# Kernel optimization log

Measured on AMD Instinct MI355X. Metric: run time of the kernel, lower is better.

Reference implementation:

```python
import jax, jax.numpy as jnp
import numpy as np

N_DOF = 7
WIDTH = 1024
BATCH = 8192
EPS = 1e-5
LSIZE = N_DOF * (N_DOF + 1) // 2   # diag (n) + strictly-lower ((n^2-n)/2)


def _tri_idx(n):
    # order matches LowTri: offset -i chunks, within-chunk j -> entry (j+i, j)
    r, c = [], []
    for i in range(n):
        for j in range(n - i):
            r.append(j + i)
            c.append(j)
    return np.array(r, np.int32), np.array(c, np.int32)

_R, _C = _tri_idx(N_DOF)


def setup_inputs() -> dict:
    key = jax.random.key(0)
    ks = jax.random.split(key, 9)

    def glorot(k, shape):
        std = (2.0 / (shape[0] + shape[1])) ** 0.5
        return (jax.random.normal(k, shape, jnp.float32) * std).astype(jnp.float32)

    lower = LSIZE - N_DOF
    b0 = 0.1
    return {
        "state": jax.random.normal(ks[0], (BATCH, N_DOF), jnp.float32),
        "velocity": jax.random.normal(ks[1], (BATCH, N_DOF), jnp.float32),
        "acceleration": jax.random.normal(ks[2], (BATCH, N_DOF), jnp.float32),
        "W_in": glorot(ks[3], (N_DOF, WIDTH)), "b_in": jnp.full((WIDTH,), b0, jnp.float32),
        "W_h": glorot(ks[4], (WIDTH, WIDTH)), "b_h": jnp.full((WIDTH,), b0, jnp.float32),
        "W_g": glorot(ks[5], (WIDTH, 1)), "b_g": jnp.full((1,), b0, jnp.float32),
        "W_ld": glorot(ks[6], (WIDTH, N_DOF)), "b_ld": jnp.full((N_DOF,), b0, jnp.float32),
        "W_lo": glorot(ks[7], (WIDTH, lower)), "b_lo": jnp.full((lower,), b0, jnp.float32),
    }


def _layer(x, der, W, b, act):
    # a: [B, out]; der: [B, in, n_dof] -> [B, out, n_dof]
    a = x @ W + b
    if act == "relu":
        y = jax.nn.relu(a)
        gp = (a > 0).astype(a.dtype)
    else:  # linear
        y = a
        gp = jnp.ones_like(a)
    # diag(g'(a)) @ W^T @ prev_der  ==  g'(a)[:, :, None] * (W^T @ prev_der)
    new_der = gp[:, :, None] * jnp.einsum("io,bid->bod", W, der)
    return y, new_der


def _forward(state, velocity, acceleration,
             W_in, b_in, W_h, b_h, W_g, b_g, W_ld, b_ld, W_lo, b_lo):
    B = state.shape[0]
    eye = jnp.broadcast_to(jnp.eye(N_DOF, dtype=state.dtype), (B, N_DOF, N_DOF))

    y1, d1 = _layer(state, eye, W_in, b_in, "relu")
    y2, d2 = _layer(y1, d1, W_h, b_h, "relu")
    y3, d3 = _layer(y2, d2, W_h, b_h, "relu")   # original reuses hidden_layer1 twice

    V, derV = _layer(y3, d3, W_g, b_g, "linear")       # derV: [B, 1, n_dof]
    l_diag, der_ld = _layer(y3, d3, W_ld, b_ld, "relu")
    l_low, der_lo = _layer(y3, d3, W_lo, b_lo, "linear")

    l = jnp.concatenate([l_diag, l_low], axis=1)          # [B, LSIZE]
    der_l = jnp.concatenate([der_ld, der_lo], axis=1)     # [B, LSIZE, n_dof]

    def lowtri(v):   # [B, LSIZE] -> [B, n, n]
        return jnp.zeros((B, N_DOF, N_DOF), v.dtype).at[:, _R, _C].set(v)

    def lowtri3d(v):  # [B, n_dof, LSIZE] -> [B, n_dof, n, n]
        return jnp.zeros((B, N_DOF, N_DOF, N_DOF), v.dtype).at[:, :, _R, _C].set(v)

    L = lowtri(l)
    LT = jnp.swapaxes(L, 1, 2)
    M = L @ LT + EPS * jnp.eye(N_DOF, dtype=L.dtype)

    dldt = jnp.einsum("bld,bd->bl", der_l, velocity)
    dLdt = lowtri(dldt)
    dMdt = L @ jnp.swapaxes(dLdt, 1, 2) + dLdt @ LT

    dLdq = lowtri3d(jnp.swapaxes(der_l, 1, 2))            # [B, n_dof, n, n]
    dMdq = dLdq @ LT[:, None] + L[:, None] @ jnp.swapaxes(dLdq, 2, 3)

    dMdt_dq = jnp.einsum("bij,bj->bi", dMdt, velocity)
    quad_dq = jnp.einsum("bi,bkij,bj->bk", velocity, dMdq, velocity)
    C = dMdt_dq - 0.5 * quad_dq
    G = derV[:, 0, :]                                      # squeeze [B,1,n_dof]
    Mddq = jnp.einsum("bij,bj->bi", M, acceleration)
    tau_pred = Mddq + C + G
    return tau_pred, M, C, G


def reference(state, velocity, acceleration,
              W_in, b_in, W_h, b_h, W_g, b_g, W_ld, b_ld, W_lo, b_lo):
    return _forward(state, velocity, acceleration,
                    W_in, b_in, W_h, b_h, W_g, b_g, W_ld, b_ld, W_lo, b_lo)
```

## Files before the change

kernel.cpp:

```cpp
#include <hip/hip_runtime.h>
#include <hip/hip_bf16.h>

#define WIDTH 1024
#define BATCH 8192

typedef __attribute__((ext_vector_type(8))) short short8;
typedef __attribute__((ext_vector_type(4))) float floatx4;

typedef __attribute__((address_space(1))) void gvoid;
typedef __attribute__((address_space(3))) void lvoid;

__device__ __forceinline__ void async_copy16(const void* g, void* l) {
    __builtin_amdgcn_global_load_lds((gvoid*)g, (lvoid*)l, 16, 0, 0);
}

__device__ __forceinline__ void split_store(float v, __hip_bfloat16* hi, __hip_bfloat16* lo, long idx) {
    __hip_bfloat16 h = __float2bfloat16(v);
    hi[idx] = h;
    lo[idx] = __float2bfloat16(v - __bfloat162float(h));
}

__global__ __launch_bounds__(256) void transpose_k(
    const float* __restrict__ W,
    __hip_bfloat16* __restrict__ Wth, __hip_bfloat16* __restrict__ Wtl)
{
    __shared__ float t[32][33];
    const int tx = threadIdx.x & 31, ty = threadIdx.x >> 5;
    const int bx = blockIdx.x << 5, by = blockIdx.y << 5;
#pragma unroll
    for (int r = 0; r < 32; r += 8)
        t[ty + r][tx] = W[(long)(by + ty + r) * WIDTH + bx + tx];
    __syncthreads();
#pragma unroll
    for (int r = 0; r < 32; r += 8)
        split_store(t[tx][ty + r], Wth, Wtl, (long)(bx + ty + r) * WIDTH + by + tx);
}

__global__ __launch_bounds__(256) void buildwcat_k(
    const float* __restrict__ W_ld, const float* __restrict__ W_lo,
    const float* __restrict__ W_g,
    __hip_bfloat16* __restrict__ Wch, __hip_bfloat16* __restrict__ Wcl)
{
    const int idx = blockIdx.x * 256 + threadIdx.x;
    const int n = idx >> 10, k = idx & 1023;
    float v = 0.f;
    if (n < 7)       v = W_ld[k * 7 + n];
    else if (n < 28) v = W_lo[k * 21 + (n - 7)];
    else if (n == 28) v = W_g[k];
    split_store(v, Wch, Wcl, idx);
}

__global__ __launch_bounds__(256) void prep_k(
    const float* __restrict__ state,
    const float* __restrict__ W_in,
    const float* __restrict__ b_in,
    __hip_bfloat16* __restrict__ Y1h, __hip_bfloat16* __restrict__ Y1l,
    __hip_bfloat16* __restrict__ D1h)
{
    const int b = blockIdx.x;
    const int j0 = threadIdx.x * 4;
    float s[7];
#pragma unroll
    for (int d = 0; d < 7; ++d) s[d] = state[b * 7 + d];
    float a[4];
#pragma unroll
    for (int q = 0; q < 4; ++q) a[q] = b_in[j0 + q];
    float w[7][4];
#pragma unroll
    for (int d = 0; d < 7; ++d)
#pragma unroll
        for (int q = 0; q < 4; ++q) {
            w[d][q] = W_in[d * WIDTH + j0 + q];
            a[q] += s[d] * w[d][q];
        }
    bool gp[4];
#pragma unroll
    for (int q = 0; q < 4; ++q) {
        gp[q] = a[q] > 0.f;
        split_store(gp[q] ? a[q] : 0.f, Y1h, Y1l, (long)b * WIDTH + j0 + q);
    }
    union { unsigned long long u64; unsigned short h[4]; } pk;
#pragma unroll
    for (int d = 0; d < 7; ++d) {
#pragma unroll
        for (int q = 0; q < 4; ++q) {
            __hip_bfloat16 v = __float2bfloat16(gp[q] ? w[d][q] : 0.f);
            pk.h[q] = *reinterpret_cast<unsigned short*>(&v);
        }
        *reinterpret_cast<unsigned long long*>(&D1h[((long)b * 7 + d) * WIDTH + j0]) = pk.u64;
    }
}

__device__ __forceinline__ void y_gemm_body(
    short* SM,
    int bm, int bn, int tid,
    const __hip_bfloat16* Ah, const __hip_bfloat16* Al,
    const __hip_bfloat16* Bh, const __hip_bfloat16* Bl,
    const float* bias,
    __hip_bfloat16* outh, __hip_bfloat16* outl)
{
    short* Ash = SM;          short* Asl = SM + 4096;
    short* Bsh = SM + 8192;   short* Bsl = SM + 12288;
    const int lane = tid & 63;
    const int wv = tid >> 6;
    const int wm = wv >> 1, wn = wv & 1;
    const int srow = tid >> 2;
    const int scol = (tid & 3) << 3;
    const short* pAh = (const short*)Ah + (long)(bm * 128 + srow) * WIDTH + scol;
    const short* pAl = (const short*)Al + (long)(bm * 128 + srow) * WIDTH + scol;
    const short* pBh = (const short*)Bh + (long)(bn * 128 + srow) * WIDTH + scol;
    const short* pBl = (const short*)Bl + (long)(bn * 128 + srow) * WIDTH + scol;
    const long half = 64l * WIDTH;

    floatx4 acc[4][4] = {};
    const int r = lane & 15;
    const int kq = (lane >> 4) << 3;

    for (int kt = 0; kt < WIDTH; kt += 32) {
        __syncthreads();
        async_copy16(pAh + kt,        Ash + wv * 512);
        async_copy16(pAh + half + kt, Ash + 2048 + wv * 512);
        async_copy16(pAl + kt,        Asl + wv * 512);
        async_copy16(pAl + half + kt, Asl + 2048 + wv * 512);
        async_copy16(pBh + kt,        Bsh + wv * 512);
        async_copy16(pBh + half + kt, Bsh + 2048 + wv * 512);
        async_copy16(pBl + kt,        Bsl + wv * 512);
        async_copy16(pBl + half + kt, Bsl + 2048 + wv * 512);
        __syncthreads();
        short8 afh[4], afl[4], bfh[4], bfl[4];
#pragma unroll
        for (int i = 0; i < 4; ++i) {
            const int ar = (wm * 64 + i * 16 + r) * 32 + kq;
            afh[i] = *reinterpret_cast<const short8*>(&Ash[ar]);
            afl[i] = *reinterpret_cast<const short8*>(&Asl[ar]);
        }
#pragma unroll
        for (int j = 0; j < 4; ++j) {
            const int br = (wn * 64 + j * 16 + r) * 32 + kq;
            bfh[j] = *reinterpret_cast<const short8*>(&Bsh[br]);
            bfl[j] = *reinterpret_cast<const short8*>(&Bsl[br]);
        }
#pragma unroll
        for (int i = 0; i < 4; ++i)
#pragma unroll
            for (int j = 0; j < 4; ++j) {
                acc[i][j] = __builtin_amdgcn_mfma_f32_16x16x32_bf16(afh[i], bfh[j], acc[i][j], 0, 0, 0);
                acc[i][j] = __builtin_amdgcn_mfma_f32_16x16x32_bf16(afh[i], bfl[j], acc[i][j], 0, 0, 0);
                acc[i][j] = __builtin_amdgcn_mfma_f32_16x16x32_bf16(afl[i], bfh[j], acc[i][j], 0, 0, 0);
            }
    }

    const int r4 = (lane >> 4) << 2;
#pragma unroll
    for (int i = 0; i < 4; ++i)
#pragma unroll
        for (int j = 0; j < 4; ++j) {
            const int col = bn * 128 + wn * 64 + j * 16 + r;
#pragma unroll
            for (int rr = 0; rr < 4; ++rr) {
                const int row = bm * 128 + wm * 64 + i * 16 + r4 + rr;
                float v = acc[i][j][rr] + bias[col];
                v = v > 0.f ? v : 0.f;
                split_store(v, outh, outl, (long)row * WIDTH + col);
            }
        }
}

__global__ __launch_bounds__(256) void gemm_y(
    const __hip_bfloat16* __restrict__ Ah, const __hip_bfloat16* __restrict__ Al,
    const __hip_bfloat16* __restrict__ Bh, const __hip_bfloat16* __restrict__ Bl,
    const float* __restrict__ bias,
    __hip_bfloat16* __restrict__ outh, __hip_bfloat16* __restrict__ outl)
{
    __shared__ __align__(16) short SM[16384];
    y_gemm_body(SM, blockIdx.x, blockIdx.y, threadIdx.x, Ah, Al, Bh, Bl, bias, outh, outl);
}


__device__ __forceinline__ void stage_chunk_d2(
    short* SMbase, const short* __restrict__ A, const short* __restrict__ B,
    int tau, int c, int tid)
{
    const short* src = (c & 1) ? B : A;
    const int kbase = (tau << 6) + ((c >> 1) << 5);
    short* region = SMbase + ((tau & 1) << 15) + (c << 13);
    const int wvb = tid & 0x1C0;
#pragma unroll
    for (int j = 0; j < 2; ++j) {
        const int idx = tid + (j << 9);
        async_copy16(src + (long)(idx >> 2) * WIDTH + kbase + ((idx & 3) << 3),
                     region + ((long)(wvb + (j << 9)) << 3));
    }
}

__global__ __launch_bounds__(512, 2) void d2y3_8p(
    const __hip_bfloat16* __restrict__ D1,
    const __hip_bfloat16* __restrict__ Wth, const __hip_bfloat16* __restrict__ Wtl,
    const __hip_bfloat16* __restrict__ Y2h, const __hip_bfloat16* __restrict__ Y2l,
    const float* __restrict__ bias,
    __hip_bfloat16* __restrict__ D2out,
    __hip_bfloat16* __restrict__ Y3h, __hip_bfloat16* __restrict__ Y3l,
    int nd2)
{
    __shared__ __align__(16) short SM[65536];
    const int tid = threadIdx.x;

    if ((int)blockIdx.x >= nd2) {
        const int half = tid >> 8;
        y_gemm_body(SM + (half << 14), blockIdx.x - nd2, blockIdx.y + (half << 2),
                    tid & 255, Y2h, Y2l, Wth, Wtl, bias, Y3h, Y3l);
        return;
    }

    const short* Abase = (const short*)D1 + (long)blockIdx.x * 256 * WIDTH;
    const short* Bbase = (const short*)Wth + (long)blockIdx.y * 256 * WIDTH;
    const int lane = tid & 63;
    const int wv = tid >> 6;
    const int wm = wv >> 2, wn = wv & 3;
    const int r = lane & 15;
    const int kq = (lane >> 4) << 3;

    floatx4 acc[8][4] = {};

    stage_chunk_d2(SM, Abase, Bbase, 0, 0, tid);
    stage_chunk_d2(SM, Abase, Bbase, 0, 1, tid);
    stage_chunk_d2(SM, Abase, Bbase, 0, 2, tid);
    stage_chunk_d2(SM, Abase, Bbase, 0, 3, tid);
    stage_chunk_d2(SM, Abase, Bbase, 1, 0, tid);
    stage_chunk_d2(SM, Abase, Bbase, 1, 1, tid);
    stage_chunk_d2(SM, Abase, Bbase, 1, 2, tid);
    asm volatile("s_waitcnt vmcnt(10)" ::: "memory");
    __builtin_amdgcn_s_barrier();

    short8 af[8], bf[2];
#pragma unroll 2
    for (int t = 0; t < 16; ++t) {
        short* buf = SM + ((t & 1) << 15);
#pragma unroll
        for (int ks = 0; ks < 2; ++ks) {
            const short* Ab = buf + (ks ? 2 : 0) * 8192;
            const short* Bb = buf + (ks ? 3 : 1) * 8192;

#pragma unroll
            for (int i = 0; i < 8; ++i)
                af[i] = *reinterpret_cast<const short8*>(&Ab[(wm * 128 + i * 16 + r) * 32 + kq]);
#pragma unroll
            for (int j = 0; j < 2; ++j)
                bf[j] = *reinterpret_cast<const short8*>(&Bb[(wn * 64 + j * 16 + r) * 32 + kq]);
            if (ks == 0) { if (t + 1 < 16) stage_chunk_d2(SM, Abase, Bbase, t + 1, 3, tid); }
            else         { if (t + 2 < 16) stage_chunk_d2(SM, Abase, Bbase, t + 2, 1, tid); }
            __builtin_amdgcn_s_barrier();
            asm volatile("s_waitcnt lgkmcnt(0)");
            __builtin_amdgcn_sched_barrier(0);
            __builtin_amdgcn_s_setprio(1);
#pragma unroll
            for (int i = 0; i < 8; ++i)
#pragma unroll
                for (int j = 0; j < 2; ++j)
                    acc[i][j] = __builtin_amdgcn_mfma_f32_16x16x32_bf16(af[i], bf[j], acc[i][j], 0, 0, 0);
            __builtin_amdgcn_s_setprio(0);
            __builtin_amdgcn_s_barrier();

#pragma unroll
            for (int j = 0; j < 2; ++j)
                bf[j] = *reinterpret_cast<const short8*>(&Bb[(wn * 64 + (2 + j) * 16 + r) * 32 + kq]);
            if (ks == 0) { if (t + 2 < 16) stage_chunk_d2(SM, Abase, Bbase, t + 2, 0, tid); }
            else         { if (t + 2 < 16) stage_chunk_d2(SM, Abase, Bbase, t + 2, 2, tid); }
            __builtin_amdgcn_s_barrier();
            asm volatile("s_waitcnt lgkmcnt(0)");
            __builtin_amdgcn_sched_barrier(0);
            __builtin_amdgcn_s_setprio(1);
#pragma unroll
            for (int i = 0; i < 8; ++i)
#pragma unroll
                for (int j = 0; j < 2; ++j)
                    acc[i][2 + j] = __builtin_amdgcn_mfma_f32_16x16x32_bf16(af[i], bf[j], acc[i][2 + j], 0, 0, 0);
            __builtin_amdgcn_s_setprio(0);
            if (ks == 0) {
                if (t < 14)       asm volatile("s_waitcnt vmcnt(10)" ::: "memory");
                else if (t == 14) asm volatile("s_waitcnt vmcnt(8)"  ::: "memory");
                else              asm volatile("s_waitcnt vmcnt(0)"  ::: "memory");
            } else {
                if (t < 14)       asm volatile("s_waitcnt vmcnt(10)" ::: "memory");
                else if (t == 14) asm volatile("s_waitcnt vmcnt(4)"  ::: "memory");
            }
            __builtin_amdgcn_s_barrier();
        }
    }

    const int r4 = (lane >> 4) << 2;
#pragma unroll
    for (int i = 0; i < 8; ++i)
#pragma unroll
        for (int j = 0; j < 4; ++j) {
            const int col = blockIdx.y * 256 + wn * 64 + j * 16 + r;
#pragma unroll
            for (int rr = 0; rr < 4; ++rr) {
                const int row = blockIdx.x * 256 + wm * 128 + i * 16 + r4 + rr;
                float v = acc[i][j][rr];
                const unsigned brow = (unsigned)row / 7u;
                if (!(__bfloat162float(Y2h[(long)brow * WIDTH + col]) > 0.f)) v = 0.f;
                D2out[(long)row * WIDTH + col] = __float2bfloat16(v);
            }
        }
}

__global__ __launch_bounds__(256) void d3heady_k(
    const __hip_bfloat16* __restrict__ D2,
    const __hip_bfloat16* __restrict__ Wth, const __hip_bfloat16* __restrict__ Wtl,
    const __hip_bfloat16* __restrict__ Y3h, const __hip_bfloat16* __restrict__ Y3l,
    const __hip_bfloat16* __restrict__ Wch, const __hip_bfloat16* __restrict__ Wcl,
    float* __restrict__ PDpart, float* __restrict__ PY,
    int nd, int Mrows)
{
    __shared__ __align__(16) short SM[26112];
    const int tid = threadIdx.x;
    const int lane = tid & 63;
    const int wv = tid >> 6;
    const int r = lane & 15;
    const int kq = (lane >> 4) << 3;
    const int r4 = (lane >> 4) << 2;
    const int srow = tid >> 2;
    const int scol = (tid & 3) << 3;
    const long half = 64l * WIDTH;

    if ((int)blockIdx.x >= nd) {
        if (blockIdx.y != 0) return;
        short* Ash = SM;          short* Asl = SM + 4096;
        short* Bsh = SM + 8192;   short* Bsl = SM + 9216;
        const int bm = blockIdx.x - nd;
        const short* pAh = (const short*)Y3h + (long)(bm * 128 + srow) * WIDTH + scol;
        const short* pAl = (const short*)Y3l + (long)(bm * 128 + srow) * WIDTH + scol;
        const long boff = (long)srow * WIDTH + scol;
        const short* pBh = (const short*)Wch;  const short* pBl = (const short*)Wcl;

        floatx4 acc[2][2] = {};
        for (int kt = 0; kt < WIDTH; kt += 32) {
            short8 gbh, gbl;
            if (tid < 128) {
                gbh = *reinterpret_cast<const short8*>(pBh + boff + kt);
                gbl = *reinterpret_cast<const short8*>(pBl + boff + kt);
            }
            __syncthreads();
            async_copy16(pAh + kt,        Ash + wv * 512);
            async_copy16(pAh + half + kt, Ash + 2048 + wv * 512);
            async_copy16(pAl + kt,        Asl + wv * 512);
            async_copy16(pAl + half + kt, Asl + 2048 + wv * 512);
            if (tid < 128) {
                *reinterpret_cast<short8*>(&Bsh[srow * 32 + scol]) = gbh;
                *reinterpret_cast<short8*>(&Bsl[srow * 32 + scol]) = gbl;
            }
            __syncthreads();
            short8 afh[2], afl[2], bfh[2], bfl[2];
#pragma unroll
            for (int i = 0; i < 2; ++i) {
                const int ar = (wv * 32 + i * 16 + r) * 32 + kq;
                afh[i] = *reinterpret_cast<const short8*>(&Ash[ar]);
                afl[i] = *reinterpret_cast<const short8*>(&Asl[ar]);
            }
#pragma unroll
            for (int j = 0; j < 2; ++j) {
                const int br = (j * 16 + r) * 32 + kq;
                bfh[j] = *reinterpret_cast<const short8*>(&Bsh[br]);
                bfl[j] = *reinterpret_cast<const short8*>(&Bsl[br]);
            }
#pragma unroll
            for (int i = 0; i < 2; ++i)
#pragma unroll
                for (int j = 0; j < 2; ++j) {
                    acc[i][j] = __builtin_amdgcn_mfma_f32_16x16x32_bf16(afh[i], bfh[j], acc[i][j], 0, 0, 0);
                    acc[i][j] = __builtin_amdgcn_mfma_f32_16x16x32_bf16(afh[i], bfl[j], acc[i][j], 0, 0, 0);
                    acc[i][j] = __builtin_amdgcn_mfma_f32_16x16x32_bf16(afl[i], bfh[j], acc[i][j], 0, 0, 0);
                }
        }
#pragma unroll
        for (int i = 0; i < 2; ++i)
#pragma unroll
            for (int j = 0; j < 2; ++j)
#pragma unroll
                for (int rr = 0; rr < 4; ++rr) {
                    const int row = bm * 128 + wv * 32 + i * 16 + r4 + rr;
                    PY[(long)row * 32 + j * 16 + r] = acc[i][j][rr];
                }
        return;
    }

    short* Ash0 = SM;         short* Ash1 = SM + 4096;
    short* Bsh0 = SM + 8192;  short* Bsh1 = SM + 12288;
    short* T    = SM;
    short* WcH  = SM + 17408;
    short* WcL  = SM + 21760;

    const int wm = wv >> 1, wn = wv & 1;
    const int bm = blockIdx.x, bn = blockIdx.y;
    const short* pAh = (const short*)D2 + (long)(bm * 128 + srow) * WIDTH + scol;
    const short* pBh = (const short*)Wth + (long)(bn * 128 + srow) * WIDTH + scol;

    floatx4 acc[4][4] = {};
    for (int kt = 0; kt < WIDTH; kt += 64) {
        __syncthreads();
        async_copy16(pAh + kt,             Ash0 + wv * 512);
        async_copy16(pAh + half + kt,      Ash0 + 2048 + wv * 512);
        async_copy16(pAh + kt + 32,        Ash1 + wv * 512);
        async_copy16(pAh + half + kt + 32, Ash1 + 2048 + wv * 512);
        async_copy16(pBh + kt,             Bsh0 + wv * 512);
        async_copy16(pBh + half + kt,      Bsh0 + 2048 + wv * 512);
        async_copy16(pBh + kt + 32,        Bsh1 + wv * 512);
        async_copy16(pBh + half + kt + 32, Bsh1 + 2048 + wv * 512);
        __syncthreads();
#pragma unroll
        for (int s = 0; s < 2; ++s) {
            const short* As = s ? Ash1 : Ash0;
            const short* Bs = s ? Bsh1 : Bsh0;
            short8 afh[4], bfh[4];
#pragma unroll
            for (int i = 0; i < 4; ++i)
                afh[i] = *reinterpret_cast<const short8*>(&As[(wm * 64 + i * 16 + r) * 32 + kq]);
#pragma unroll
            for (int j = 0; j < 4; ++j)
                bfh[j] = *reinterpret_cast<const short8*>(&Bs[(wn * 64 + j * 16 + r) * 32 + kq]);
#pragma unroll
            for (int i = 0; i < 4; ++i)
#pragma unroll
                for (int j = 0; j < 4; ++j)
                    acc[i][j] = __builtin_amdgcn_mfma_f32_16x16x32_bf16(afh[i], bfh[j], acc[i][j], 0, 0, 0);
        }
    }

    __syncthreads();
#pragma unroll
    for (int i = 0; i < 4; ++i)
#pragma unroll
        for (int j = 0; j < 4; ++j) {
            const int coll = wn * 64 + j * 16 + r;
            const int colg = bn * 128 + coll;
#pragma unroll
            for (int rr = 0; rr < 4; ++rr) {
                const int rowl = wm * 64 + i * 16 + r4 + rr;
                const int rowg = bm * 128 + rowl;
                float v = acc[i][j][rr];
                const unsigned brow = (unsigned)rowg / 7u;
                if (!(__bfloat162float(Y3h[(long)brow * WIDTH + colg]) > 0.f)) v = 0.f;
                __hip_bfloat16 hb = __float2bfloat16(v);
                T[rowl * 136 + coll] = *reinterpret_cast<short*>(&hb);
            }
        }
    {
        const int n = tid >> 4, k8 = (tid & 15) * 8;
        const short* wh = (const short*)Wch;
        const short* wl = (const short*)Wcl;
        *reinterpret_cast<short8*>(&WcH[n * 136 + k8]) =
            *reinterpret_cast<const short8*>(wh + n * WIDTH + bn * 128 + k8);
        *reinterpret_cast<short8*>(&WcH[(n + 16) * 136 + k8]) =
            *reinterpret_cast<const short8*>(wh + (n + 16) * WIDTH + bn * 128 + k8);
        *reinterpret_cast<short8*>(&WcL[n * 136 + k8]) =
            *reinterpret_cast<const short8*>(wl + n * WIDTH + bn * 128 + k8);
        *reinterpret_cast<short8*>(&WcL[(n + 16) * 136 + k8]) =
            *reinterpret_cast<const short8*>(wl + (n + 16) * WIDTH + bn * 128 + k8);
    }
    __syncthreads();

    floatx4 accp[2][2] = {};
#pragma unroll
    for (int kk = 0; kk < 128; kk += 32) {
        short8 af[2], bh8[2], bl8[2];
#pragma unroll
        for (int i = 0; i < 2; ++i)
            af[i] = *reinterpret_cast<const short8*>(&T[(wv * 32 + i * 16 + r) * 136 + kk + kq]);
#pragma unroll
        for (int j = 0; j < 2; ++j) {
            bh8[j] = *reinterpret_cast<const short8*>(&WcH[(j * 16 + r) * 136 + kk + kq]);
            bl8[j] = *reinterpret_cast<const short8*>(&WcL[(j * 16 + r) * 136 + kk + kq]);
        }
#pragma unroll
        for (int i = 0; i < 2; ++i)
#pragma unroll
            for (int j = 0; j < 2; ++j) {
                accp[i][j] = __builtin_amdgcn_mfma_f32_16x16x32_bf16(af[i], bh8[j], accp[i][j], 0, 0, 0);
                accp[i][j] = __builtin_amdgcn_mfma_f32_16x16x32_bf16(af[i], bl8[j], accp[i][j], 0, 0, 0);
            }
    }
#pragma unroll
    for (int i = 0; i < 2; ++i)
#pragma unroll
        for (int j = 0; j < 2; ++j)
#pragma unroll
            for (int rr = 0; rr < 4; ++rr) {
                const int rowg = bm * 128 + wv * 32 + i * 16 + r4 + rr;
                PDpart[((long)bn * Mrows + rowg) * 32 + j * 16 + r] = accp[i][j][rr];
            }
}

__device__ __forceinline__ int midx(int rr, int cc) {
    const int i = rr - cc;
    return i * 7 - (i * (i - 1)) / 2 + cc;
}

__global__ __launch_bounds__(64) void finalize_k(
    const float* __restrict__ PY,
    const float* __restrict__ PDpart,
    const float* __restrict__ vel_g,
    const float* __restrict__ acc_g,
    const float* __restrict__ b_ld,
    const float* __restrict__ b_lo,
    float* __restrict__ out,
    int b0, int Mrows)
{
    __shared__ float lval[28];
    __shared__ int gpv[7];
    __shared__ float derl[29 * 7];
    __shared__ float Lm[49], Mm[49], dLt[49], uu[49];
    __shared__ float wvv[7], pv[7], Cv[7], Gv[7], tauv[7], vl[7], ac[7];

    const int bl = blockIdx.x, tid = threadIdx.x;
    const int b = b0 + bl;
    if (tid < 28) {
        float s = PY[(long)bl * 32 + tid];
        if (tid < 7) {
            s += b_ld[tid];
            gpv[tid] = s > 0.f;
            lval[tid] = s > 0.f ? s : 0.f;
        } else {
            lval[tid] = s + b_lo[tid - 7];
        }
    }
    if (tid >= 28 && tid < 35) {
        vl[tid - 28] = vel_g[b * 7 + tid - 28];
        ac[tid - 28] = acc_g[b * 7 + tid - 28];
    }
    __syncthreads();
    for (int idx = tid; idx < 203; idx += 64) {
        const int m = idx / 7, d = idx % 7;
        float v = 0.f;
#pragma unroll
        for (int p = 0; p < 8; ++p)
            v += PDpart[((long)p * Mrows + bl * 7 + d) * 32 + m];
        if (m < 7 && !gpv[m]) v = 0.f;
        derl[m * 7 + d] = v;
    }
    __syncthreads();
    if (tid < 49) {
        const int rr = tid / 7, cc = tid % 7;
        Lm[tid] = (rr >= cc) ? lval[midx(rr, cc)] : 0.f;
    }
    __syncthreads();
    if (tid < 49) {
        const int rr = tid / 7, cc = tid % 7;
        float s = 0.f;
        for (int k = 0; k < 7; ++k) s += Lm[rr * 7 + k] * Lm[cc * 7 + k];
        if (rr == cc) s += 1e-5f;
        Mm[tid] = s;
        float t = 0.f;
        if (rr >= cc) {
            const int m = midx(rr, cc);
            for (int d = 0; d < 7; ++d) t += derl[m * 7 + d] * vl[d];
        }
        dLt[tid] = t;
        float u = 0.f;
        for (int r2 = cc; r2 < 7; ++r2) u += vl[r2] * derl[midx(r2, cc) * 7 + rr];
        uu[tid] = u;
    } else if (tid >= 49 && tid < 56) {
        const int j = tid - 49;
        float s = 0.f;
        for (int r2 = 0; r2 < 7; ++r2) s += Lm[r2 * 7 + j] * vl[r2];
        wvv[j] = s;
    }
    __syncthreads();
    if (tid < 7) {
        float s = 0.f;
        for (int r2 = 0; r2 < 7; ++r2) s += dLt[r2 * 7 + tid] * vl[r2];
        pv[tid] = s;
    }
    __syncthreads();
    if (tid < 7) {
        float s = 0.f, q = 0.f, md = 0.f;
        for (int c = 0; c < 7; ++c) {
            s += Lm[tid * 7 + c] * pv[c] + dLt[tid * 7 + c] * wvv[c];
            q += uu[tid * 7 + c] * wvv[c];
            md += Mm[tid * 7 + c] * ac[c];
        }
        Cv[tid] = s - q;
        Gv[tid] = derl[28 * 7 + tid];
        tauv[tid] = md + Cv[tid] + Gv[tid];
    }
    __syncthreads();
    if (tid < 49) out[57344 + (long)b * 49 + tid] = Mm[tid];
    if (tid < 7) {
        out[(long)b * 7 + tid] = tauv[tid];
        out[458752 + (long)b * 7 + tid] = Cv[tid];
        out[516096 + (long)b * 7 + tid] = Gv[tid];
    }
}

extern "C" void kernel_launch(void* const* d_in, const int* in_sizes, int n_in,
                              void* d_out, int out_size, void* d_ws, size_t ws_size,
                              hipStream_t stream)
{
    const float* state = (const float*)d_in[0];
    const float* vel   = (const float*)d_in[1];
    const float* accel = (const float*)d_in[2];
    const float* W_in  = (const float*)d_in[3];
    const float* b_in  = (const float*)d_in[4];
    const float* W_h   = (const float*)d_in[5];
    const float* b_h   = (const float*)d_in[6];
    const float* W_g   = (const float*)d_in[7];
    const float* W_ld  = (const float*)d_in[9];
    const float* b_ld  = (const float*)d_in[10];
    const float* W_lo  = (const float*)d_in[11];
    const float* b_lo  = (const float*)d_in[12];
    float* outp = (float*)d_out;

    char* ws = (char*)d_ws;
    __hip_bfloat16* Wth = (__hip_bfloat16*)ws; ws += (size_t)WIDTH * WIDTH * 2;
    __hip_bfloat16* Wtl = (__hip_bfloat16*)ws; ws += (size_t)WIDTH * WIDTH * 2;
    __hip_bfloat16* Wch = (__hip_bfloat16*)ws; ws += 32 * WIDTH * 2;
    __hip_bfloat16* Wcl = (__hip_bfloat16*)ws; ws += 32 * WIDTH * 2;
    const size_t fixed = (size_t)(ws - (char*)d_ws);

    int CH = 256;
    for (int cand = 8192; cand >= 256; cand >>= 1) {
        size_t need = fixed + (size_t)cand * 37120;
        if (need <= ws_size) { CH = cand; break; }
    }
    const int NCH = BATCH / CH;

    const size_t YB = (size_t)CH * WIDTH * 2;
    const size_t DB = (size_t)CH * 7 * WIDTH * 2;
    __hip_bfloat16* Yah = (__hip_bfloat16*)ws; ws += YB;
    __hip_bfloat16* Yal = (__hip_bfloat16*)ws; ws += YB;
    __hip_bfloat16* Ybh = (__hip_bfloat16*)ws; ws += YB;
    __hip_bfloat16* Ybl = (__hip_bfloat16*)ws; ws += YB;
    __hip_bfloat16* Dah = (__hip_bfloat16*)ws; ws += DB;
    __hip_bfloat16* Dbh = (__hip_bfloat16*)ws; ws += DB;
    float* PY = (float*)ws; ws += (size_t)CH * 32 * 4;
    float* PDpart = (float*)Dah;

    const int Mrows = CH * 7;
    const int nd = Mrows / 128;
    const int ny = CH / 128;
    const int nd2 = Mrows / 256;

    transpose_k<<<dim3(32, 32), dim3(256), 0, stream>>>(W_h, Wth, Wtl);
    buildwcat_k<<<dim3(128), dim3(256), 0, stream>>>(W_ld, W_lo, W_g, Wch, Wcl);

    for (int c = 0; c < NCH; ++c) {
        prep_k<<<dim3(CH), dim3(256), 0, stream>>>(state + (size_t)c * CH * 7, W_in, b_in,
                                                   Yah, Yal, Dah);
        gemm_y<<<dim3(ny, 8), dim3(256), 0, stream>>>(
            Yah, Yal, Wth, Wtl, b_h, Ybh, Ybl);
        d2y3_8p<<<dim3(nd2 + ny, 4), dim3(512), 0, stream>>>(
            Dah, Wth, Wtl, Ybh, Ybl, b_h, Dbh, Yah, Yal, nd2);
        d3heady_k<<<dim3(nd + ny, 8), dim3(256), 0, stream>>>(
            Dbh, Wth, Wtl, Yah, Yal, Wch, Wcl, PDpart, PY, nd, Mrows);
        finalize_k<<<dim3(CH), dim3(64), 0, stream>>>(PY, PDpart, vel, accel, b_ld, b_lo,
                                                      outp, c * CH, Mrows);
    }
    (void)in_sizes; (void)n_in; (void)out_size;
}
```

Measured before the change: 671.6 us.

## Pipeline Y GEMMs with 512-thread double-buffered tiles and merge D3 into 256-row kernel

Replaces the 256-thread Y GEMM with a 512-thread, 128x256 tile body that double-buffers hi/lo operand chunks in LDS using async loads, explicit vmcnt waits, barriers and setprio around MFMA groups. The D3 derivative GEMM reuses the deeper 256-row pipelined D2 GEMM path, which halves the number of partial PD slices that finalize must sum. The head GEMM is split into two halves per 512-thread block. The aim is to hide global-to-LDS latency and raise MFMA utilisation. The cost is more LDS per block and hand-tuned wait counts that are fragile.

```diff
diff --git a/kernel.cpp b/kernel.cpp
--- a/kernel.cpp
+++ b/kernel.cpp
@@ -18,6 +18,16 @@
     __hip_bfloat16 h = __float2bfloat16(v);
     hi[idx] = h;
     lo[idx] = __float2bfloat16(v - __bfloat162float(h));
+}
+
+template<int N> __device__ __forceinline__ void waitv() {
+    if constexpr (N == 0)      asm volatile("s_waitcnt vmcnt(0)" ::: "memory");
+    else if constexpr (N == 1) asm volatile("s_waitcnt vmcnt(1)" ::: "memory");
+    else if constexpr (N == 3) asm volatile("s_waitcnt vmcnt(3)" ::: "memory");
+    else if constexpr (N == 6) asm volatile("s_waitcnt vmcnt(6)" ::: "memory");
+    else if constexpr (N == 7) asm volatile("s_waitcnt vmcnt(7)" ::: "memory");
+    else if constexpr (N == 8) asm volatile("s_waitcnt vmcnt(8)" ::: "memory");
+    else if constexpr (N == 9) asm volatile("s_waitcnt vmcnt(9)" ::: "memory");
 }
 
 __global__ __launch_bounds__(256) void transpose_k(
@@ -91,71 +101,122 @@
     }
 }
 
-__device__ __forceinline__ void y_gemm_body(
+
+__device__ __forceinline__ void st128(const short* src, short* region, int tid, int kbase) {
+    async_copy16(src + (long)(tid >> 2) * WIDTH + kbase + ((tid & 3) << 3),
+                 region + ((tid & 0x1C0) << 3));
+}
+__device__ __forceinline__ void st256(const short* src, short* region, int tid, int kbase) {
+#pragma unroll
+    for (int j = 0; j < 2; ++j) {
+        const int idx = tid + (j << 9);
+        async_copy16(src + (long)(idx >> 2) * WIDTH + kbase + ((idx & 3) << 3),
+                     region + (((tid & 0x1C0) + (j << 9)) << 3));
+    }
+}
+
+template<int W0, int W1, int W2, int IS>
+__device__ __forceinline__ void y8_triple(
+    short* buf, short* nbuf,
+    const short* pAh, const short* pAl, const short* pBh, const short* pBl,
+    int t, int tid, int wm, int wn, int r, int kq, floatx4 (&acc)[4][4])
+{
+    short8 fah[4], fbh[4];
+#pragma unroll
+    for (int i = 0; i < 4; ++i)
+        fah[i] = *reinterpret_cast<const short8*>(&buf[(wm * 64 + i * 16 + r) * 32 + kq]);
+#pragma unroll
+    for (int j = 0; j < 4; ++j)
+        fbh[j] = *reinterpret_cast<const short8*>(&buf[8192 + (wn * 64 + j * 16 + r) * 32 + kq]);
+    if (IS >= 1) st128(pAl, nbuf + 4096, tid, (t + 1) * 32);
+    __builtin_amdgcn_s_barrier();
+    asm volatile("s_waitcnt lgkmcnt(0)");
+    __builtin_amdgcn_sched_barrier(0);
+    __builtin_amdgcn_s_setprio(1);
+#pragma unroll
+    for (int i = 0; i < 4; ++i)
+#pragma unroll
+        for (int j = 0; j < 4; ++j)
+            acc[i][j] = __builtin_amdgcn_mfma_f32_16x16x32_bf16(fah[i], fbh[j], acc[i][j], 0, 0, 0);
+    __builtin_amdgcn_s_setprio(0);
+    waitv<W0>();
+    __builtin_amdgcn_s_barrier();
+    short8 fbl[4];
+#pragma unroll
+    for (int j = 0; j < 4; ++j)
+        fbl[j] = *reinterpret_cast<const short8*>(&buf[16384 + (wn * 64 + j * 16 + r) * 32 + kq]);
+    if (IS >= 2) { st128(pAh, buf, tid, (t + 2) * 32); st256(pBh, buf + 8192, tid, (t + 2) * 32); }
+    __builtin_amdgcn_s_barrier();
+    asm volatile("s_waitcnt lgkmcnt(0)");
+    __builtin_amdgcn_sched_barrier(0);
+    __builtin_amdgcn_s_setprio(1);
+#pragma unroll
+    for (int i = 0; i < 4; ++i)
+#pragma unroll
+        for (int j = 0; j < 4; ++j)
+            acc[i][j] = __builtin_amdgcn_mfma_f32_16x16x32_bf16(fah[i], fbl[j], acc[i][j], 0, 0, 0);
+    __builtin_amdgcn_s_setprio(0);
+    waitv<W1>();
+    __builtin_amdgcn_s_barrier();
+    short8 fal[4];
+#pragma unroll
+    for (int i = 0; i < 4; ++i)
+        fal[i] = *reinterpret_cast<const short8*>(&buf[4096 + (wm * 64 + i * 16 + r) * 32 + kq]);
+    if (IS >= 2) st256(pBl, buf + 16384, tid, (t + 2) * 32);
+    __builtin_amdgcn_s_barrier();
+    asm volatile("s_waitcnt lgkmcnt(0)");
+    __builtin_amdgcn_sched_barrier(0);
+    __builtin_amdgcn_s_setprio(1);
+#pragma unroll
+    for (int i = 0; i < 4; ++i)
+#pragma unroll
+        for (int j = 0; j < 4; ++j)
+            acc[i][j] = __builtin_amdgcn_mfma_f32_16x16x32_bf16(fal[i], fbh[j], acc[i][j], 0, 0, 0);
+    __builtin_amdgcn_s_setprio(0);
+    waitv<W2>();
+    __builtin_amdgcn_s_barrier();
+}
+
+__device__ __forceinline__ void y8_gemm_body(
     short* SM,
     int bm, int bn, int tid,
-    const __hip_bfloat16* Ah, const __hip_bfloat16* Al,
-    const __hip_bfloat16* Bh, const __hip_bfloat16* Bl,
+    const __hip_bfloat16* Ah_, const __hip_bfloat16* Al_,
+    const __hip_bfloat16* Bh_, const __hip_bfloat16* Bl_,
     const float* bias,
     __hip_bfloat16* outh, __hip_bfloat16* outl)
 {
-    short* Ash = SM;          short* Asl = SM + 4096;
-    short* Bsh = SM + 8192;   short* Bsl = SM + 12288;
-    const int lane = tid & 63;
-    const int wv = tid >> 6;
-    const int wm = wv >> 1, wn = wv & 1;
-    const int srow = tid >> 2;
-    const int scol = (tid & 3) << 3;
-    const short* pAh = (const short*)Ah + (long)(bm * 128 + srow) * WIDTH + scol;
-    const short* pAl = (const short*)Al + (long)(bm * 128 + srow) * WIDTH + scol;
-    const short* pBh = (const short*)Bh + (long)(bn * 128 + srow) * WIDTH + scol;
-    const short* pBl = (const short*)Bl + (long)(bn * 128 + srow) * WIDTH + scol;
-    const long half = 64l * WIDTH;
+    const int lane = tid & 63, wv = tid >> 6;
+    const int wm = wv >> 2, wn = wv & 3;
+    const int r = lane & 15, kq = (lane >> 4) << 3, r4 = (lane >> 4) << 2;
+    const short* pAh = (const short*)Ah_ + (long)bm * 128 * WIDTH;
+    const short* pAl = (const short*)Al_ + (long)bm * 128 * WIDTH;
+    const short* pBh = (const short*)Bh_ + (long)bn * 256 * WIDTH;
+    const short* pBl = (const short*)Bl_ + (long)bn * 256 * WIDTH;
 
     floatx4 acc[4][4] = {};
-    const int r = lane & 15;
-    const int kq = (lane >> 4) << 3;
-
-    for (int kt = 0; kt < WIDTH; kt += 32) {
-        __syncthreads();
-        async_copy16(pAh + kt,        Ash + wv * 512);
-        async_copy16(pAh + half + kt, Ash + 2048 + wv * 512);
-        async_copy16(pAl + kt,        Asl + wv * 512);
-        async_copy16(pAl + half + kt, Asl + 2048 + wv * 512);
-        async_copy16(pBh + kt,        Bsh + wv * 512);
-        async_copy16(pBh + half + kt, Bsh + 2048 + wv * 512);
-        async_copy16(pBl + kt,        Bsl + wv * 512);
-        async_copy16(pBl + half + kt, Bsl + 2048 + wv * 512);
-        __syncthreads();
-        short8 afh[4], afl[4], bfh[4], bfl[4];
-#pragma unroll
-        for (int i = 0; i < 4; ++i) {
-            const int ar = (wm * 64 + i * 16 + r) * 32 + kq;
-            afh[i] = *reinterpret_cast<const short8*>(&Ash[ar]);
-            afl[i] = *reinterpret_cast<const short8*>(&Asl[ar]);
-        }
+
+    st128(pAh, SM + 0,     tid, 0);
+    st256(pBh, SM + 8192,  tid, 0);
+    st256(pBl, SM + 16384, tid, 0);
+    st128(pAl, SM + 4096,  tid, 0);
+    st128(pAh, SM + 24576 + 0,     tid, 32);
+    st256(pBh, SM + 24576 + 8192,  tid, 32);
+    st256(pBl, SM + 24576 + 16384, tid, 32);
+    waitv<8>();
+    __builtin_amdgcn_s_barrier();
+
+    for (int t2 = 0; t2 < 15; ++t2) {
+        y8_triple<7, 9, 8, 2>(SM,         SM + 24576, pAh, pAl, pBh, pBl, 2 * t2,     tid, wm, wn, r, kq, acc);
+        y8_triple<7, 9, 8, 2>(SM + 24576, SM,         pAh, pAl, pBh, pBl, 2 * t2 + 1, tid, wm, wn, r, kq, acc);
+    }
+    y8_triple<7, 6, 3, 1>(SM,         SM + 24576, pAh, pAl, pBh, pBl, 30, tid, wm, wn, r, kq, acc);
+    y8_triple<1, 0, 0, 0>(SM + 24576, SM,         pAh, pAl, pBh, pBl, 31, tid, wm, wn, r, kq, acc);
+
+#pragma unroll
+    for (int i = 0; i < 4; ++i)
 #pragma unroll
         for (int j = 0; j < 4; ++j) {
-            const int br = (wn * 64 + j * 16 + r) * 32 + kq;
-            bfh[j] = *reinterpret_cast<const short8*>(&Bsh[br]);
-            bfl[j] = *reinterpret_cast<const short8*>(&Bsl[br]);
-        }
-#pragma unroll
-        for (int i = 0; i < 4; ++i)
-#pragma unroll
-            for (int j = 0; j < 4; ++j) {
-                acc[i][j] = __builtin_amdgcn_mfma_f32_16x16x32_bf16(afh[i], bfh[j], acc[i][j], 0, 0, 0);
-                acc[i][j] = __builtin_amdgcn_mfma_f32_16x16x32_bf16(afh[i], bfl[j], acc[i][j], 0, 0, 0);
-                acc[i][j] = __builtin_amdgcn_mfma_f32_16x16x32_bf16(afl[i], bfh[j], acc[i][j], 0, 0, 0);
-            }
-    }
-
-    const int r4 = (lane >> 4) << 2;
-#pragma unroll
-    for (int i = 0; i < 4; ++i)
-#pragma unroll
-        for (int j = 0; j < 4; ++j) {
-            const int col = bn * 128 + wn * 64 + j * 16 + r;
+            const int col = bn * 256 + wn * 64 + j * 16 + r;
 #pragma unroll
             for (int rr = 0; rr < 4; ++rr) {
                 const int row = bm * 128 + wm * 64 + i * 16 + r4 + rr;
@@ -166,16 +227,15 @@
         }
 }
 
-__global__ __launch_bounds__(256) void gemm_y(
+__global__ __launch_bounds__(512, 2) void gemm_y8(
     const __hip_bfloat16* __restrict__ Ah, const __hip_bfloat16* __restrict__ Al,
     const __hip_bfloat16* __restrict__ Bh, const __hip_bfloat16* __restrict__ Bl,
     const float* __restrict__ bias,
     __hip_bfloat16* __restrict__ outh, __hip_bfloat16* __restrict__ outl)
 {
-    __shared__ __align__(16) short SM[16384];
-    y_gemm_body(SM, blockIdx.x, blockIdx.y, threadIdx.x, Ah, Al, Bh, Bl, bias, outh, outl);
-}
-
+    __shared__ __align__(16) short SM[49152];
+    y8_gemm_body(SM, blockIdx.x, blockIdx.y, threadIdx.x, Ah, Al, Bh, Bl, bias, outh, outl);
+}
 
 __device__ __forceinline__ void stage_chunk_d2(
     short* SMbase, const short* __restrict__ A, const short* __restrict__ B,
@@ -193,35 +253,10 @@
     }
 }
 
-__global__ __launch_bounds__(512, 2) void d2y3_8p(
-    const __hip_bfloat16* __restrict__ D1,
-    const __hip_bfloat16* __restrict__ Wth, const __hip_bfloat16* __restrict__ Wtl,
-    const __hip_bfloat16* __restrict__ Y2h, const __hip_bfloat16* __restrict__ Y2l,
-    const float* __restrict__ bias,
-    __hip_bfloat16* __restrict__ D2out,
-    __hip_bfloat16* __restrict__ Y3h, __hip_bfloat16* __restrict__ Y3l,
-    int nd2)
-{
-    __shared__ __align__(16) short SM[65536];
-    const int tid = threadIdx.x;
-
-    if ((int)blockIdx.x >= nd2) {
-        const int half = tid >> 8;
-        y_gemm_body(SM + (half << 14), blockIdx.x - nd2, blockIdx.y + (half << 2),
-                    tid & 255, Y2h, Y2l, Wth, Wtl, bias, Y3h, Y3l);
-        return;
-    }
-
-    const short* Abase = (const short*)D1 + (long)blockIdx.x * 256 * WIDTH;
-    const short* Bbase = (const short*)Wth + (long)blockIdx.y * 256 * WIDTH;
-    const int lane = tid & 63;
-    const int wv = tid >> 6;
-    const int wm = wv >> 2, wn = wv & 3;
-    const int r = lane & 15;
-    const int kq = (lane >> 4) << 3;
-
-    floatx4 acc[8][4] = {};
-
+__device__ __forceinline__ void d_gemm_256(
+    short* SM, const short* Abase, const short* Bbase, int tid,
+    int wm, int wn, int r, int kq, floatx4 (&acc)[8][4])
+{
     stage_chunk_d2(SM, Abase, Bbase, 0, 0, tid);
     stage_chunk_d2(SM, Abase, Bbase, 0, 1, tid);
     stage_chunk_d2(SM, Abase, Bbase, 0, 2, tid);
@@ -287,6 +322,33 @@
             __builtin_amdgcn_s_barrier();
         }
     }
+}
+
+__global__ __launch_bounds__(512, 2) void d2y3_8p(
+    const __hip_bfloat16* __restrict__ D1,
+    const __hip_bfloat16* __restrict__ Wth, const __hip_bfloat16* __restrict__ Wtl,
+    const __hip_bfloat16* __restrict__ Y2h, const __hip_bfloat16* __restrict__ Y2l,
+    const float* __restrict__ bias,
+    __hip_bfloat16* __restrict__ D2out,
+    __hip_bfloat16* __restrict__ Y3h, __hip_bfloat16* __restrict__ Y3l,
+    int nd2)
+{
+    __shared__ __align__(16) short SM[65536];
+    const int tid = threadIdx.x;
+
+    if ((int)blockIdx.x >= nd2) {
+        y8_gemm_body(SM, blockIdx.x - nd2, blockIdx.y, tid, Y2h, Y2l, Wth, Wtl, bias, Y3h, Y3l);
+        return;
+    }
+
+    const short* Abase = (const short*)D1 + (long)blockIdx.x * 256 * WIDTH;
+    const short* Bbase = (const short*)Wth + (long)blockIdx.y * 256 * WIDTH;
+    const int lane = tid & 63, wv = tid >> 6;
+    const int wm = wv >> 2, wn = wv & 3;
+    const int r = lane & 15, kq = (lane >> 4) << 3;
+
+    floatx4 acc[8][4] = {};
+    d_gemm_256(SM, Abase, Bbase, tid, wm, wn, r, kq, acc);
 
     const int r4 = (lane >> 4) << 2;
 #pragma unroll
@@ -305,188 +367,166 @@
         }
 }
 
-__global__ __launch_bounds__(256) void d3heady_k(
+__device__ __forceinline__ void heady_half(
+    short* SMh, int bm, int tl,
+    const __hip_bfloat16* __restrict__ Y3h, const __hip_bfloat16* __restrict__ Y3l,
+    const __hip_bfloat16* __restrict__ Wch, const __hip_bfloat16* __restrict__ Wcl,
+    float* __restrict__ PY)
+{
+    short* Ash = SMh;          short* Asl = SMh + 4096;
+    short* Bsh = SMh + 8192;   short* Bsl = SMh + 9216;
+    const int lane = tl & 63;
+    const int wv = tl >> 6;
+    const int r = lane & 15, kq = (lane >> 4) << 3, r4 = (lane >> 4) << 2;
+    const int srow = tl >> 2, scol = (tl & 3) << 3;
+    const long half = 64l * WIDTH;
+    const short* pAh = (const short*)Y3h + (long)(bm * 128 + srow) * WIDTH + scol;
+    const short* pAl = (const short*)Y3l + (long)(bm * 128 + srow) * WIDTH + scol;
+    const long boff = (long)srow * WIDTH + scol;
+    const short* pBh = (const short*)Wch;  const short* pBl = (const short*)Wcl;
+
+    floatx4 acc[2][2] = {};
+    for (int kt = 0; kt < WIDTH; kt += 32) {
+        short8 gbh, gbl;
+        if (tl < 128) {
+            gbh = *reinterpret_cast<const short8*>(pBh + boff + kt);
+            gbl = *reinterpret_cast<const short8*>(pBl + boff + kt);
+        }
+        __syncthreads();
+        async_copy16(pAh + kt,        Ash + wv * 512);
+        async_copy16(pAh + half + kt, Ash + 2048 + wv * 512);
+        async_copy16(pAl + kt,        Asl + wv * 512);
+        async_copy16(pAl + half + kt, Asl + 2048 + wv * 512);
+        if (tl < 128) {
+            *reinterpret_cast<short8*>(&Bsh[srow * 32 + scol]) = gbh;
+            *reinterpret_cast<short8*>(&Bsl[srow * 32 + scol]) = gbl;
+        }
+        __syncthreads();
+        short8 afh[2], afl[2], bfh[2], bfl[2];
+#pragma unroll
+        for (int i = 0; i < 2; ++i) {
+            const int ar = (wv * 32 + i * 16 + r) * 32 + kq;
+            afh[i] = *reinterpret_cast<const short8*>(&Ash[ar]);
+            afl[i] = *reinterpret_cast<const short8*>(&Asl[ar]);
+        }
+#pragma unroll
+        for (int j = 0; j < 2; ++j) {
+            const int br = (j * 16 + r) * 32 + kq;
+            bfh[j] = *reinterpret_cast<const short8*>(&Bsh[br]);
+            bfl[j] = *reinterpret_cast<const short8*>(&Bsl[br]);
+        }
+#pragma unroll
+        for (int i = 0; i < 2; ++i)
+#pragma unroll
+            for (int j = 0; j < 2; ++j) {
+                acc[i][j] = __builtin_amdgcn_mfma_f32_16x16x32_bf16(afh[i], bfh[j], acc[i][j], 0, 0, 0);
+                acc[i][j] = __builtin_amdgcn_mfma_f32_16x16x32_bf16(afh[i], bfl[j], acc[i][j], 0, 0, 0);
+                acc[i][j] = __builtin_amdgcn_mfma_f32_16x16x32_bf16(afl[i], bfh[j], acc[i][j], 0, 0, 0);
+            }
+    }
+#pragma unroll
+    for (int i = 0; i < 2; ++i)
+#pragma unroll
+        for (int j = 0; j < 2; ++j)
+#pragma unroll
+            for (int rr = 0; rr < 4; ++rr) {
+                const int row = bm * 128 + wv * 32 + i * 16 + r4 + rr;
+                PY[(long)row * 32 + j * 16 + r] = acc[i][j][rr];
+            }
+}
+
+__global__ __launch_bounds__(512, 2) void d3pd_8p(
     const __hip_bfloat16* __restrict__ D2,
     const __hip_bfloat16* __restrict__ Wth, const __hip_bfloat16* __restrict__ Wtl,
     const __hip_bfloat16* __restrict__ Y3h, const __hip_bfloat16* __restrict__ Y3l,
     const __hip_bfloat16* __restrict__ Wch, const __hip_bfloat16* __restrict__ Wcl,
     float* __restrict__ PDpart, float* __restrict__ PY,
-    int nd, int Mrows)
-{
-    __shared__ __align__(16) short SM[26112];
+    int nd2, int Mrows)
+{
+    __shared__ __align__(16) short SM[65536];
     const int tid = threadIdx.x;
-    const int lane = tid & 63;
-    const int wv = tid >> 6;
-    const int r = lane & 15;
-    const int kq = (lane >> 4) << 3;
-    const int r4 = (lane >> 4) << 2;
-    const int srow = tid >> 2;
-    const int scol = (tid & 3) << 3;
-    const long half = 64l * WIDTH;
-
-    if ((int)blockIdx.x >= nd) {
+
+    if ((int)blockIdx.x >= nd2) {
         if (blockIdx.y != 0) return;
-        short* Ash = SM;          short* Asl = SM + 4096;
-        short* Bsh = SM + 8192;   short* Bsl = SM + 9216;
-        const int bm = blockIdx.x - nd;
-        const short* pAh = (const short*)Y3h + (long)(bm * 128 + srow) * WIDTH + scol;
-        const short* pAl = (const short*)Y3l + (long)(bm * 128 + srow) * WIDTH + scol;
-        const long boff = (long)srow * WIDTH + scol;
-        const short* pBh = (const short*)Wch;  const short* pBl = (const short*)Wcl;
-
-        floatx4 acc[2][2] = {};
-        for (int kt = 0; kt < WIDTH; kt += 32) {
-            short8 gbh, gbl;
-            if (tid < 128) {
-                gbh = *reinterpret_cast<const short8*>(pBh + boff + kt);
-                gbl = *reinterpret_cast<const short8*>(pBl + boff + kt);
+        const int hd = (blockIdx.x - nd2) * 2 + (tid >> 8);
+        heady_half(SM + (tid >> 8) * 10240, hd, tid & 255, Y3h, Y3l, Wch, Wcl, PY);
+        return;
+    }
+
+    const int lane = tid & 63, wv = tid >> 6;
+    const int wm = wv >> 2, wn = wv & 3;
+    const int r = lane & 15, kq = (lane >> 4) << 3, r4 = (lane >> 4) << 2;
+    const int bm = blockIdx.x, bn = blockIdx.y;
+    const short* Abase = (const short*)D2 + (long)bm * 256 * WIDTH;
+    const short* Bbase = (const short*)Wth + (long)bn * 256 * WIDTH;
+
+    floatx4 acc[8][4] = {};
+    d_gemm_256(SM, Abase, Bbase, tid, wm, wn, r, kq, acc);
+
+    short* T   = SM;
+    short* WcH = SM + 34816;
+    short* WcL = SM + 39168;
+
+    floatx4 accp[2][2] = {};
+#pragma unroll
+    for (int h = 0; h < 2; ++h) {
+        __syncthreads();
+        if ((wn >> 1) == h) {
+#pragma unroll
+            for (int i = 0; i < 8; ++i)
+#pragma unroll
+                for (int j = 0; j < 4; ++j) {
+                    const int ct = (wn & 1) * 64 + j * 16 + r;
+                    const int colg = bn * 256 + h * 128 + ct;
+#pragma unroll
+                    for (int rr = 0; rr < 4; ++rr) {
+                        const int rowl = wm * 128 + i * 16 + r4 + rr;
+                        const int rowg = bm * 256 + rowl;
+                        float v = acc[i][j][rr];
+                        const unsigned brow = (unsigned)rowg / 7u;
+                        if (!(__bfloat162float(Y3h[(long)brow * WIDTH + colg]) > 0.f)) v = 0.f;
+                        __hip_bfloat16 hb = __float2bfloat16(v);
+                        T[rowl * 136 + ct] = *reinterpret_cast<short*>(&hb);
+                    }
+                }
+        }
+        {
+            const int n = tid >> 4, k8 = (tid & 15) * 8;
+            const short* wh = (const short*)Wch;
+            const short* wl = (const short*)Wcl;
+            *reinterpret_cast<short8*>(&WcH[n * 136 + k8]) =
+                *reinterpret_cast<const short8*>(wh + (long)n * WIDTH + bn * 256 + h * 128 + k8);
+            *reinterpret_cast<short8*>(&WcL[n * 136 + k8]) =
+                *reinterpret_cast<const short8*>(wl + (long)n * WIDTH + bn * 256 + h * 128 + k8);
+        }
+        __syncthreads();
+#pragma unroll
+        for (int kk = 0; kk < 128; kk += 32) {
+            short8 af2[2], bh8[2], bl8[2];
+#pragma unroll
+            for (int i = 0; i < 2; ++i)
+                af2[i] = *reinterpret_cast<const short8*>(&T[(wv * 32 + i * 16 + r) * 136 + kk + kq]);
+#pragma unroll
+            for (int j = 0; j < 2; ++j) {
+                bh8[j] = *reinterpret_cast<const short8*>(&WcH[(j * 16 + r) * 136 + kk + kq]);
+                bl8[j] = *reinterpret_cast<const short8*>(&WcL[(j * 16 + r) * 136 + kk + kq]);
             }
-            __syncthreads();
-            async_copy16(pAh + kt,        Ash + wv * 512);
-            async_copy16(pAh + half + kt, Ash + 2048 + wv * 512);
-            async_copy16(pAl + kt,        Asl + wv * 512);
-            async_copy16(pAl + half + kt, Asl + 2048 + wv * 512);
-            if (tid < 128) {
-                *reinterpret_cast<short8*>(&Bsh[srow * 32 + scol]) = gbh;
-                *reinterpret_cast<short8*>(&Bsl[srow * 32 + scol]) = gbl;
-            }
-            __syncthreads();
-            short8 afh[2], afl[2], bfh[2], bfl[2];
-#pragma unroll
-            for (int i = 0; i < 2; ++i) {
-                const int ar = (wv * 32 + i * 16 + r) * 32 + kq;
-                afh[i] = *reinterpret_cast<const short8*>(&Ash[ar]);
-                afl[i] = *reinterpret_cast<const short8*>(&Asl[ar]);
-            }
-#pragma unroll
-            for (int j = 0; j < 2; ++j) {
-                const int br = (j * 16 + r) * 32 + kq;
-                bfh[j] = *reinterpret_cast<const short8*>(&Bsh[br]);
-                bfl[j] = *reinterpret_cast<const short8*>(&Bsl[br]);
-            }
 #pragma unroll
             for (int i = 0; i < 2; ++i)
 #pragma unroll
                 for (int j = 0; j < 2; ++j) {
-                    acc[i][j] = __builtin_amdgcn_mfma_f32_16x16x32_bf16(afh[i], bfh[j], acc[i][j], 0, 0, 0);
-                    acc[i][j] = __builtin_amdgcn_mfma_f32_16x16x32_bf16(afh[i], bfl[j], acc[i][j], 0, 0, 0);
-                    acc[i][j] = __builtin_amdgcn_mfma_f32_16x16x32_bf16(afl[i], bfh[j], acc[i][j], 0, 0, 0);
+                    accp[i][j] = __builtin_amdgcn_mfma_f32_16x16x32_bf16(af2[i], bh8[j], accp[i][j], 0, 0, 0);
+                    accp[i][j] = __builtin_amdgcn_mfma_f32_16x16x32_bf16(af2[i], bl8[j], accp[i][j], 0, 0, 0);
                 }
         }
-#pragma unroll
-        for (int i = 0; i < 2; ++i)
-#pragma unroll
-            for (int j = 0; j < 2; ++j)
-#pragma unroll
-                for (int rr = 0; rr < 4; ++rr) {
-                    const int row = bm * 128 + wv * 32 + i * 16 + r4 + rr;
-                    PY[(long)row * 32 + j * 16 + r] = acc[i][j][rr];
-                }
-        return;
-    }
-
-    short* Ash0 = SM;         short* Ash1 = SM + 4096;
-    short* Bsh0 = SM + 8192;  short* Bsh1 = SM + 12288;
-    short* T    = SM;
-    short* WcH  = SM + 17408;
-    short* WcL  = SM + 21760;
-
-    const int wm = wv >> 1, wn = wv & 1;
-    const int bm = blockIdx.x, bn = blockIdx.y;
-    const short* pAh = (const short*)D2 + (long)(bm * 128 + srow) * WIDTH + scol;
-    const short* pBh = (const short*)Wth + (long)(bn * 128 + srow) * WIDTH + scol;
-
-    floatx4 acc[4][4] = {};
-    for (int kt = 0; kt < WIDTH; kt += 64) {
-        __syncthreads();
-        async_copy16(pAh + kt,             Ash0 + wv * 512);
-        async_copy16(pAh + half + kt,      Ash0 + 2048 + wv * 512);
-        async_copy16(pAh + kt + 32,        Ash1 + wv * 512);
-        async_copy16(pAh + half + kt + 32, Ash1 + 2048 + wv * 512);
-        async_copy16(pBh + kt,             Bsh0 + wv * 512);
-        async_copy16(pBh + half + kt,      Bsh0 + 2048 + wv * 512);
-        async_copy16(pBh + kt + 32,        Bsh1 + wv * 512);
-        async_copy16(pBh + half + kt + 32, Bsh1 + 2048 + wv * 512);
-        __syncthreads();
-#pragma unroll
-        for (int s = 0; s < 2; ++s) {
-            const short* As = s ? Ash1 : Ash0;
-            const short* Bs = s ? Bsh1 : Bsh0;
-            short8 afh[4], bfh[4];
-#pragma unroll
-            for (int i = 0; i < 4; ++i)
-                afh[i] = *reinterpret_cast<const short8*>(&As[(wm * 64 + i * 16 + r) * 32 + kq]);
-#pragma unroll
-            for (int j = 0; j < 4; ++j)
-                bfh[j] = *reinterpret_cast<const short8*>(&Bs[(wn * 64 + j * 16 + r) * 32 + kq]);
-#pragma unroll
-            for (int i = 0; i < 4; ++i)
-#pragma unroll
-                for (int j = 0; j < 4; ++j)
-                    acc[i][j] = __builtin_amdgcn_mfma_f32_16x16x32_bf16(afh[i], bfh[j], acc[i][j], 0, 0, 0);
-        }
-    }
-
-    __syncthreads();
-#pragma unroll
-    for (int i = 0; i < 4; ++i)
-#pragma unroll
-        for (int j = 0; j < 4; ++j) {
-            const int coll = wn * 64 + j * 16 + r;
-            const int colg = bn * 128 + coll;
+    }
+#pragma unroll
+    for (int i = 0; i < 2; ++i)
+#pragma unroll
+        for (int j = 0; j < 2; ++j)
 #pragma unroll
             for (int rr = 0; rr < 4; ++rr) {
-                const int rowl = wm * 64 + i * 16 + r4 + rr;
-                const int rowg = bm * 128 + rowl;
-                float v = acc[i][j][rr];
-                const unsigned brow = (unsigned)rowg / 7u;
-                if (!(__bfloat162float(Y3h[(long)brow * WIDTH + colg]) > 0.f)) v = 0.f;
-                __hip_bfloat16 hb = __float2bfloat16(v);
-                T[rowl * 136 + coll] = *reinterpret_cast<short*>(&hb);
-            }
-        }
-    {
-        const int n = tid >> 4, k8 = (tid & 15) * 8;
-        const short* wh = (const short*)Wch;
-        const short* wl = (const short*)Wcl;
-        *reinterpret_cast<short8*>(&WcH[n * 136 + k8]) =
-            *reinterpret_cast<const short8*>(wh + n * WIDTH + bn * 128 + k8);
-        *reinterpret_cast<short8*>(&WcH[(n + 16) * 136 + k8]) =
-            *reinterpret_cast<const short8*>(wh + (n + 16) * WIDTH + bn * 128 + k8);
-        *reinterpret_cast<short8*>(&WcL[n * 136 + k8]) =
-            *reinterpret_cast<const short8*>(wl + n * WIDTH + bn * 128 + k8);
-        *reinterpret_cast<short8*>(&WcL[(n + 16) * 136 + k8]) =
-            *reinterpret_cast<const short8*>(wl + (n + 16) * WIDTH + bn * 128 + k8);
-    }
-    __syncthreads();
-
-    floatx4 accp[2][2] = {};
-#pragma unroll
-    for (int kk = 0; kk < 128; kk += 32) {
-        short8 af[2], bh8[2], bl8[2];
-#pragma unroll
-        for (int i = 0; i < 2; ++i)
-            af[i] = *reinterpret_cast<const short8*>(&T[(wv * 32 + i * 16 + r) * 136 + kk + kq]);
-#pragma unroll
-        for (int j = 0; j < 2; ++j) {
-            bh8[j] = *reinterpret_cast<const short8*>(&WcH[(j * 16 + r) * 136 + kk + kq]);
-            bl8[j] = *reinterpret_cast<const short8*>(&WcL[(j * 16 + r) * 136 + kk + kq]);
-        }
-#pragma unroll
-        for (int i = 0; i < 2; ++i)
-#pragma unroll
-            for (int j = 0; j < 2; ++j) {
-                accp[i][j] = __builtin_amdgcn_mfma_f32_16x16x32_bf16(af[i], bh8[j], accp[i][j], 0, 0, 0);
-                accp[i][j] = __builtin_amdgcn_mfma_f32_16x16x32_bf16(af[i], bl8[j], accp[i][j], 0, 0, 0);
-            }
-    }
-#pragma unroll
-    for (int i = 0; i < 2; ++i)
-#pragma unroll
-        for (int j = 0; j < 2; ++j)
-#pragma unroll
-            for (int rr = 0; rr < 4; ++rr) {
-                const int rowg = bm * 128 + wv * 32 + i * 16 + r4 + rr;
+                const int rowg = bm * 256 + wv * 32 + i * 16 + r4 + rr;
                 PDpart[((long)bn * Mrows + rowg) * 32 + j * 16 + r] = accp[i][j][rr];
             }
 }
@@ -533,7 +573,7 @@
         const int m = idx / 7, d = idx % 7;
         float v = 0.f;
 #pragma unroll
-        for (int p = 0; p < 8; ++p)
+        for (int p = 0; p < 4; ++p)
             v += PDpart[((long)p * Mrows + bl * 7 + d) * 32 + m];
         if (m < 7 && !gpv[m]) v = 0.f;
         derl[m * 7 + d] = v;
@@ -636,9 +676,8 @@
     float* PDpart = (float*)Dah;
 
     const int Mrows = CH * 7;
-    const int nd = Mrows / 128;
-    const int ny = CH / 128;
     const int nd2 = Mrows / 256;
+    const int ny128 = CH / 128;
 
     transpose_k<<<dim3(32, 32), dim3(256), 0, stream>>>(W_h, Wth, Wtl);
     buildwcat_k<<<dim3(128), dim3(256), 0, stream>>>(W_ld, W_lo, W_g, Wch, Wcl);
@@ -646,12 +685,12 @@
     for (int c = 0; c < NCH; ++c) {
         prep_k<<<dim3(CH), dim3(256), 0, stream>>>(state + (size_t)c * CH * 7, W_in, b_in,
                                                    Yah, Yal, Dah);
-        gemm_y<<<dim3(ny, 8), dim3(256), 0, stream>>>(
+        gemm_y8<<<dim3(ny128, 4), dim3(512), 0, stream>>>(
             Yah, Yal, Wth, Wtl, b_h, Ybh, Ybl);
-        d2y3_8p<<<dim3(nd2 + ny, 4), dim3(512), 0, stream>>>(
+        d2y3_8p<<<dim3(nd2 + ny128, 4), dim3(512), 0, stream>>>(
             Dah, Wth, Wtl, Ybh, Ybl, b_h, Dbh, Yah, Yal, nd2);
-        d3heady_k<<<dim3(nd + ny, 8), dim3(256), 0, stream>>>(
-            Dbh, Wth, Wtl, Yah, Yal, Wch, Wcl, PDpart, PY, nd, Mrows);
+        d3pd_8p<<<dim3(nd2 + ny128 / 2, 4), dim3(512), 0, stream>>>(
+            Dbh, Wth, Wtl, Yah, Yal, Wch, Wcl, PDpart, PY, nd2, Mrows);
         finalize_k<<<dim3(CH), dim3(64), 0, stream>>>(PY, PDpart, vel, accel, b_ld, b_lo,
                                                       outp, c * CH, Mrows);
     }
```

Result: faster. 618.5 us (-7.9%).
